# Kernel tuning notes

Hardware: AMD Instinct MI355X
Metric: run time of the kernel (lower is better)

The kernel has to match this reference:

```python
import jax, jax.numpy as jnp
import numpy as np

BUCKETS = 256
B, CIN, H, W = 16, 64, 128, 128
COUT, K = 64, 3


def setup_inputs() -> dict:
    key = jax.random.key(0)
    k1, k2, k3, k4, k5 = jax.random.split(key, 5)
    x = jax.random.normal(k1, (B, CIN, H, W), dtype=jnp.float32)
    x_hash = jax.random.normal(k2, (B, CIN, H, W), dtype=jnp.float32)
    conv_weight = jax.random.normal(k3, (COUT, CIN, K, K), dtype=jnp.float32)
    hash_value = jnp.sort(jax.random.normal(k4, (BUCKETS,), dtype=jnp.float32))
    bias = jax.random.normal(k5, (COUT,), dtype=jnp.float32) * 0.1
    return {"x": x, "x_hash": x_hash, "conv_weight": conv_weight,
            "hash_value": hash_value, "bias": bias}


def _conv(x, w, b):
    # stride 1, padding 1 -> same spatial size (matches nn.Conv2d(padding=1))
    y = jax.lax.conv_general_dilated(
        x, w, window_strides=(1, 1), padding=[(1, 1), (1, 1)],
        dimension_numbers=("NCHW", "OIHW", "NCHW"))
    return y + b[None, :, None, None]


def _hash_weights(conv_weight, hash_value):
    # Uniform bucketization of weights into BUCKETS bins over [min, max],
    # then gather of the learned per-bucket hash value.
    w_min = jnp.min(conv_weight)
    w_max = jnp.max(conv_weight)
    width = (w_max - w_min) / BUCKETS
    idx = jnp.floor((conv_weight - w_min) / width).astype(jnp.int32)
    # w == max floors to BUCKETS; torch code assigns it the last bucket.
    idx = jnp.clip(idx, 0, BUCKETS - 1)
    return jnp.take(hash_value, idx)


def reference(x, x_hash, conv_weight, hash_value, bias):
    hash_weight = _hash_weights(conv_weight, hash_value)
    out = _conv(x, conv_weight, bias)
    hash_out = _conv(x, hash_weight, bias)
    out_hash = _conv(x_hash, hash_weight, bias)
    return (out, hash_out, out_hash)
```

## Files before the change

### kernel.cpp

```cpp
#include <hip/hip_runtime.h>
#include <stdint.h>

typedef short short8_t __attribute__((ext_vector_type(8)));
typedef unsigned short ushort2_t __attribute__((ext_vector_type(2)));
typedef float f32x4    __attribute__((ext_vector_type(4)));

__device__ __forceinline__ unsigned short f2bf(float f) {
  unsigned int u = __float_as_uint(f);
  u += 0x7FFFu + ((u >> 16) & 1u);
  return (unsigned short)(u >> 16);
}

__device__ __forceinline__ void glld16(const void* src, char* lds) {
  __builtin_amdgcn_global_load_lds(
      (const __attribute__((address_space(1))) void*)src,
      (__attribute__((address_space(3))) void*)lds, 16, 0, 0);
}

__device__ __forceinline__ short8_t lds_rd(const char* smem, int a) {
  int aa = a ^ (((a >> 7) & 7) << 4);
  return *(const short8_t*)(smem + aa);
}

__global__ __launch_bounds__(256) void minmax_kernel(const float* __restrict__ w,
                                                     float* __restrict__ mm) {
  int tid = threadIdx.x;
  float mn = 1e30f, mx = -1e30f;
  const float4* w4 = (const float4*)w;
  for (int i = tid; i < 9216; i += 256) {
    float4 v = w4[i];
    mn = fminf(mn, fminf(fminf(v.x, v.y), fminf(v.z, v.w)));
    mx = fmaxf(mx, fmaxf(fmaxf(v.x, v.y), fmaxf(v.z, v.w)));
  }
  for (int off = 32; off; off >>= 1) {
    mn = fminf(mn, __shfl_down(mn, off));
    mx = fmaxf(mx, __shfl_down(mx, off));
  }
  __shared__ float smn[4], smx[4];
  if ((tid & 63) == 0) { smn[tid >> 6] = mn; smx[tid >> 6] = mx; }
  __syncthreads();
  if (tid == 0) {
    mn = fminf(fminf(smn[0], smn[1]), fminf(smn[2], smn[3]));
    mx = fmaxf(fmaxf(smx[0], smx[1]), fmaxf(smx[2], smx[3]));
    mm[0] = mn; mm[1] = mx;
  }
}

__global__ __launch_bounds__(256) void hashprep_kernel(const float* __restrict__ w,
                                                       const float* __restrict__ hv,
                                                       const float* __restrict__ mm,
                                                       unsigned short* __restrict__ w0,
                                                       unsigned short* __restrict__ w1) {
  int t = blockIdx.x * 256 + threadIdx.x;
  if (t >= 36864) return;
  float mn = mm[0], mx = mm[1];
  float width = (mx - mn) / 256.0f;
  float wv = w[t];
  int idx = min(max((int)floorf((wv - mn) / width), 0), 255);
  float hw = hv[idx];
  int co  = t / 576;
  int rem = t - co * 576;
  int ci  = rem / 9;
  int tap = rem - ci * 9;
  int mt = co >> 4, m = co & 15;
  int ks = ci >> 5, g = (ci & 31) >> 3, e = ci & 7;
  int dst = ((tap * 8 + mt * 2 + ks) * 64 + g * 16 + m) * 8 + e;
  w0[dst] = f2bf(wv);
  w1[dst] = f2bf(hw);
}

__global__ __launch_bounds__(256) void xprep_kernel(const float* __restrict__ x,
                                                    unsigned short* __restrict__ xbf) {
  __shared__ unsigned short T[64 * 130];
  int t  = threadIdx.x;
  int bh = blockIdx.x;
  int b = bh >> 7, h = bh & 127;
  const f32x4* x4 = (const f32x4*)x;
  size_t xrow = (((size_t)(b * 64) * 128 + h) << 5);
  #pragma unroll
  for (int k = 0; k < 8; ++k) {
    int j = k * 256 + t;
    int c = j >> 5, w4 = j & 31;
    f32x4 v = x4[xrow + ((size_t)c << 12) + w4];
    ushort2_t lo, hi;
    lo[0] = f2bf(v[0]); lo[1] = f2bf(v[1]);
    hi[0] = f2bf(v[2]); hi[1] = f2bf(v[3]);
    *(ushort2_t*)&T[c * 130 + w4 * 4]     = lo;
    *(ushort2_t*)&T[c * 130 + w4 * 4 + 2] = hi;
  }
  __syncthreads();
  size_t rb = (size_t)bh * (130 * 64);
  if (t < 16) {
    short8_t z = {0, 0, 0, 0, 0, 0, 0, 0};
    int col = (t < 8) ? 0 : 129, ch = t & 7;
    *(short8_t*)(xbf + rb + col * 64 + ch * 8) = z;
  }
  #pragma unroll
  for (int k = 0; k < 4; ++k) {
    int q = k * 256 + t;
    int w = q >> 3, o8 = (q & 7) * 8;
    short8_t v;
    #pragma unroll
    for (int j = 0; j < 8; ++j) v[j] = (short)T[(o8 + j) * 130 + w];
    *(short8_t*)(xbf + rb + (size_t)(w + 1) * 64 + o8) = v;
  }
}

#define XR 8448

template<int NSETS>
__global__ __launch_bounds__(256, 2) void conv_kernel(
    const unsigned short* __restrict__ xbf,
    const char* __restrict__ zeropage,
    const unsigned short* __restrict__ wf0,
    const unsigned short* __restrict__ wf1,
    const float* __restrict__ bias,
    float* __restrict__ out0,
    float* __restrict__ out1) {

  __shared__ char smem[6 * XR];

  int tid = threadIdx.x, lane = tid & 63, wv = tid >> 6;
  int m = lane & 15, g = lane >> 4;

  int bx0 = blockIdx.x;
  int bx  = (bx0 & 7) * 128 + (bx0 >> 3);
  int b = bx >> 6, rowblk = (bx >> 1) & 31, wblk = bx & 1;
  int h0 = rowblk * 4, W0 = wblk * 64;

  const unsigned short* wsrc[2] = {wf0, wf1};

  short8_t aw[NSETS][8];
  #pragma unroll
  for (int s = 0; s < NSETS; ++s)
    #pragma unroll
    for (int i = 0; i < 8; ++i)
      aw[s][i] = *(const short8_t*)(wsrc[s] + i * 512 + lane * 8);

  const char* xb = (const char*)xbf + (size_t)b * (130 * 128 * 128) + (size_t)W0 * 128;
  for (int batch = wv; batch < 50; batch += 4) {
    int q = batch * 64 + lane;
    if (q < 3168) {
      int r = q / 528;
      int o = (q - r * 528) << 4;
      int swz = o ^ (((q >> 3) & 7) << 4);
      int hin = h0 + r - 1;
      const char* src = ((unsigned)hin < 128u) ? (xb + (size_t)hin * 16640 + swz)
                                               : (zeropage + swz);
      glld16(src, smem + batch * 1024);
    }
  }

  f32x4 acc[NSETS][4][4];
  #pragma unroll
  for (int s = 0; s < NSETS; ++s)
    #pragma unroll
    for (int i = 0; i < 4; ++i)
      #pragma unroll
      for (int j = 0; j < 4; ++j) acc[s][i][j] = (f32x4){0.f, 0.f, 0.f, 0.f};

  int bcol[4];
  #pragma unroll
  for (int nf = 0; nf < 4; ++nf) bcol[nf] = ((nf * 16 + m) << 7) + (g << 4);

  __syncthreads();

  #pragma unroll
  for (int t = 0; t < 9; ++t) {
    if (t) {
      #pragma unroll
      for (int s = 0; s < NSETS; ++s)
        #pragma unroll
        for (int i = 0; i < 8; ++i)
          aw[s][i] = *(const short8_t*)(wsrc[s] + t * 4096 + i * 512 + lane * 8);
    }
    int kh = t / 3, kw = t - kh * 3;
    int xtap = (wv + kh) * XR + (kw << 7);
    #pragma unroll
    for (int ks = 0; ks < 2; ++ks) {
      short8_t bf[4];
      #pragma unroll
      for (int nf = 0; nf < 4; ++nf) bf[nf] = lds_rd(smem, xtap + bcol[nf] + (ks << 6));
      #pragma unroll
      for (int s = 0; s < NSETS; ++s)
        #pragma unroll
        for (int mt = 0; mt < 4; ++mt)
          #pragma unroll
          for (int nf = 0; nf < 4; ++nf)
            acc[s][mt][nf] = __builtin_amdgcn_mfma_f32_16x16x32_bf16(
                aw[s][mt * 2 + ks], bf[nf], acc[s][mt][nf], 0, 0, 0);
    }
  }

  size_t ob = (size_t)b * 64 * 16384 + (size_t)(h0 + wv) * 128 + W0;
  #pragma unroll
  for (int s = 0; s < NSETS; ++s) {
    float* op = s ? out1 : out0;
    #pragma unroll
    for (int mt = 0; mt < 4; ++mt)
      #pragma unroll
      for (int r4 = 0; r4 < 4; ++r4) {
        int co = mt * 16 + g * 4 + r4;
        float bv = bias[co];
        #pragma unroll
        for (int nf = 0; nf < 4; ++nf)
          op[ob + (size_t)co * 16384 + nf * 16 + m] = acc[s][mt][nf][r4] + bv;
      }
  }
}

extern "C" void kernel_launch(void* const* d_in, const int* in_sizes, int n_in,
                              void* d_out, int out_size, void* d_ws, size_t ws_size,
                              hipStream_t stream) {
  const float* x    = (const float*)d_in[0];
  const float* xh   = (const float*)d_in[1];
  const float* cw   = (const float*)d_in[2];
  const float* hv   = (const float*)d_in[3];
  const float* bias = (const float*)d_in[4];

  float* out      = (float*)d_out;
  float* hash_out = out + 16777216;
  float* out_hash = out + 33554432;

  char* ws = (char*)d_ws;
  float* mm            = (float*)ws;
  char* zeropage       = ws + 128;
  unsigned short* w0F  = (unsigned short*)(ws + 32768);
  unsigned short* w1F  = (unsigned short*)(ws + 32768 + 73728);
  unsigned short* xbf  = (unsigned short*)(ws + 180224);

  hipMemsetAsync(zeropage, 0, 16640, stream);
  minmax_kernel<<<1, 256, 0, stream>>>(cw, mm);
  hashprep_kernel<<<144, 256, 0, stream>>>(cw, hv, mm, w0F, w1F);

  xprep_kernel<<<2048, 256, 0, stream>>>(x, xbf);
  conv_kernel<2><<<1024, 256, 0, stream>>>(xbf, zeropage, w0F, w1F, bias, out, hash_out);
  xprep_kernel<<<2048, 256, 0, stream>>>(xh, xbf);
  conv_kernel<1><<<1024, 256, 0, stream>>>(xbf, zeropage, w1F, w1F, bias, out_hash, out_hash);
}
```

Baseline: 392.0 us.

## Merge conv launches, use 32x32x16 MFMA, and swizzle the xprep transpose

Both inputs are converted in a single xprep launch into separate bf16 buffers, and one conv launch of 2048 blocks covers both passes, with each block choosing two weight sets or one. The MFMA tile changes from 16x16x32 to 32x32x16, and the weight fragment layout is rebuilt to match. The xprep transpose now uses an XOR-swizzled LDS tile with packed channel pairs and vector reads. This removes two launches and the serial dependency between the passes, and should cut LDS operand reads per MFMA. The cost is extra workspace for a second bf16 buffer, uneven work across blocks, and possible register-pressure changes from the runtime branch on the number of weight sets.

```diff
diff --git a/kernel.cpp b/kernel.cpp
--- a/kernel.cpp
+++ b/kernel.cpp
@@ -2,8 +2,8 @@
 #include <stdint.h>
 
 typedef short short8_t __attribute__((ext_vector_type(8)));
-typedef unsigned short ushort2_t __attribute__((ext_vector_type(2)));
 typedef float f32x4    __attribute__((ext_vector_type(4)));
+typedef float f32x16   __attribute__((ext_vector_type(16)));
 
 __device__ __forceinline__ unsigned short f2bf(float f) {
   unsigned int u = __float_as_uint(f);
@@ -62,82 +62,102 @@
   int rem = t - co * 576;
   int ci  = rem / 9;
   int tap = rem - ci * 9;
-  int mt = co >> 4, m = co & 15;
-  int ks = ci >> 5, g = (ci & 31) >> 3, e = ci & 7;
-  int dst = ((tap * 8 + mt * 2 + ks) * 64 + g * 16 + m) * 8 + e;
+  int mt = co >> 5, m = co & 31;
+  int ks = ci >> 4, k = ci & 15;
+  int f = mt * 4 + ks;
+  int lane = (k >> 3) * 32 + m;
+  int dst = ((tap * 8 + f) * 64 + lane) * 8 + (k & 7);
   w0[dst] = f2bf(wv);
   w1[dst] = f2bf(hw);
 }
 
 __global__ __launch_bounds__(256) void xprep_kernel(const float* __restrict__ x,
-                                                    unsigned short* __restrict__ xbf) {
-  __shared__ unsigned short T[64 * 130];
-  int t  = threadIdx.x;
-  int bh = blockIdx.x;
+                                                    const float* __restrict__ xh,
+                                                    unsigned short* __restrict__ xbf,
+                                                    unsigned short* __restrict__ xhbf) {
+  __shared__ unsigned short T[128 * 64];
+  int t   = threadIdx.x;
+  int bid = blockIdx.x;
+  int which = bid >> 11;
+  int bh = bid & 2047;
+  const float* src = which ? xh : x;
+  unsigned short* dst = which ? xhbf : xbf;
   int b = bh >> 7, h = bh & 127;
-  const f32x4* x4 = (const f32x4*)x;
+  const f32x4* x4 = (const f32x4*)src;
   size_t xrow = (((size_t)(b * 64) * 128 + h) << 5);
   #pragma unroll
-  for (int k = 0; k < 8; ++k) {
-    int j = k * 256 + t;
-    int c = j >> 5, w4 = j & 31;
-    f32x4 v = x4[xrow + ((size_t)c << 12) + w4];
-    ushort2_t lo, hi;
-    lo[0] = f2bf(v[0]); lo[1] = f2bf(v[1]);
-    hi[0] = f2bf(v[2]); hi[1] = f2bf(v[3]);
-    *(ushort2_t*)&T[c * 130 + w4 * 4]     = lo;
-    *(ushort2_t*)&T[c * 130 + w4 * 4 + 2] = hi;
+  for (int kk = 0; kk < 4; ++kk) {
+    int j = kk * 256 + t;
+    int c2 = j >> 5, w4 = j & 31;
+    int c = c2 * 2;
+    f32x4 v0 = x4[xrow + ((size_t)c << 12) + w4];
+    f32x4 v1 = x4[xrow + ((size_t)(c + 1) << 12) + w4];
+    int cs = c ^ ((w4 & 7) << 3);
+    #pragma unroll
+    for (int jj = 0; jj < 4; ++jj) {
+      int w = w4 * 4 + jj;
+      unsigned int pk = (unsigned int)f2bf(v0[jj]) | ((unsigned int)f2bf(v1[jj]) << 16);
+      *(unsigned int*)&T[w * 64 + cs] = pk;
+    }
   }
   __syncthreads();
   size_t rb = (size_t)bh * (130 * 64);
   if (t < 16) {
     short8_t z = {0, 0, 0, 0, 0, 0, 0, 0};
     int col = (t < 8) ? 0 : 129, ch = t & 7;
-    *(short8_t*)(xbf + rb + col * 64 + ch * 8) = z;
-  }
-  #pragma unroll
-  for (int k = 0; k < 4; ++k) {
-    int q = k * 256 + t;
-    int w = q >> 3, o8 = (q & 7) * 8;
-    short8_t v;
-    #pragma unroll
-    for (int j = 0; j < 8; ++j) v[j] = (short)T[(o8 + j) * 130 + w];
-    *(short8_t*)(xbf + rb + (size_t)(w + 1) * 64 + o8) = v;
+    *(short8_t*)(dst + rb + col * 64 + ch * 8) = z;
+  }
+  #pragma unroll
+  for (int kk = 0; kk < 4; ++kk) {
+    int q = kk * 256 + t;
+    int w = q >> 3, c0 = (q & 7) * 8;
+    int cs0 = c0 ^ (((w >> 2) & 7) << 3);
+    short8_t v = *(const short8_t*)&T[w * 64 + cs0];
+    *(short8_t*)(dst + rb + (size_t)(w + 1) * 64 + c0) = v;
   }
 }
 
 #define XR 8448
 
-template<int NSETS>
 __global__ __launch_bounds__(256, 2) void conv_kernel(
     const unsigned short* __restrict__ xbf,
+    const unsigned short* __restrict__ xhbf,
     const char* __restrict__ zeropage,
     const unsigned short* __restrict__ wf0,
     const unsigned short* __restrict__ wf1,
     const float* __restrict__ bias,
     float* __restrict__ out0,
-    float* __restrict__ out1) {
+    float* __restrict__ out1,
+    float* __restrict__ out2) {
 
   __shared__ char smem[6 * XR];
 
   int tid = threadIdx.x, lane = tid & 63, wv = tid >> 6;
-  int m = lane & 15, g = lane >> 4;
+  int nlo = lane & 31, hi = lane >> 5;
 
   int bx0 = blockIdx.x;
-  int bx  = (bx0 & 7) * 128 + (bx0 >> 3);
-  int b = bx >> 6, rowblk = (bx >> 1) & 31, wblk = bx & 1;
+  int bx  = (bx0 & 7) * 256 + (bx0 >> 3);
+  int which = bx >> 10;
+  int r10 = bx & 1023;
+  int b = r10 >> 6, rowblk = (r10 >> 1) & 31, wblk = r10 & 1;
   int h0 = rowblk * 4, W0 = wblk * 64;
-
-  const unsigned short* wsrc[2] = {wf0, wf1};
-
-  short8_t aw[NSETS][8];
-  #pragma unroll
-  for (int s = 0; s < NSETS; ++s)
+  int nsets = 2 - which;
+
+  const unsigned short* xsrc  = which ? xhbf : xbf;
+  const unsigned short* wsrc0 = which ? wf1 : wf0;
+  float* o0 = which ? out2 : out0;
+
+  short8_t aw0[8], aw1[8];
+  #pragma unroll
+  for (int i = 0; i < 8; ++i)
+    aw0[i] = *(const short8_t*)(wsrc0 + i * 512 + lane * 8);
+  if (nsets == 2) {
     #pragma unroll
     for (int i = 0; i < 8; ++i)
-      aw[s][i] = *(const short8_t*)(wsrc[s] + i * 512 + lane * 8);
-
-  const char* xb = (const char*)xbf + (size_t)b * (130 * 128 * 128) + (size_t)W0 * 128;
+      aw1[i] = *(const short8_t*)(wf1 + i * 512 + lane * 8);
+  }
+
+  const char* xb = (const char*)xsrc + (size_t)b * (130 * 128 * 128) + (size_t)W0 * 128;
   for (int batch = wv; batch < 50; batch += 4) {
     int q = batch * 64 + lane;
     if (q < 3168) {
@@ -151,17 +171,14 @@
     }
   }
 
-  f32x4 acc[NSETS][4][4];
-  #pragma unroll
-  for (int s = 0; s < NSETS; ++s)
-    #pragma unroll
-    for (int i = 0; i < 4; ++i)
-      #pragma unroll
-      for (int j = 0; j < 4; ++j) acc[s][i][j] = (f32x4){0.f, 0.f, 0.f, 0.f};
-
-  int bcol[4];
-  #pragma unroll
-  for (int nf = 0; nf < 4; ++nf) bcol[nf] = ((nf * 16 + m) << 7) + (g << 4);
+  f32x16 acc0[2][2], acc1[2][2];
+  #pragma unroll
+  for (int i = 0; i < 2; ++i)
+    #pragma unroll
+    for (int j = 0; j < 2; ++j) {
+      #pragma unroll
+      for (int e = 0; e < 16; ++e) { acc0[i][j][e] = 0.f; acc1[i][j][e] = 0.f; }
+    }
 
   __syncthreads();
 
@@ -169,43 +186,59 @@
   for (int t = 0; t < 9; ++t) {
     if (t) {
       #pragma unroll
-      for (int s = 0; s < NSETS; ++s)
+      for (int i = 0; i < 8; ++i)
+        aw0[i] = *(const short8_t*)(wsrc0 + t * 4096 + i * 512 + lane * 8);
+      if (nsets == 2) {
         #pragma unroll
         for (int i = 0; i < 8; ++i)
-          aw[s][i] = *(const short8_t*)(wsrc[s] + t * 4096 + i * 512 + lane * 8);
+          aw1[i] = *(const short8_t*)(wf1 + t * 4096 + i * 512 + lane * 8);
+      }
     }
     int kh = t / 3, kw = t - kh * 3;
-    int xtap = (wv + kh) * XR + (kw << 7);
-    #pragma unroll
-    for (int ks = 0; ks < 2; ++ks) {
-      short8_t bf[4];
-      #pragma unroll
-      for (int nf = 0; nf < 4; ++nf) bf[nf] = lds_rd(smem, xtap + bcol[nf] + (ks << 6));
-      #pragma unroll
-      for (int s = 0; s < NSETS; ++s)
-        #pragma unroll
-        for (int mt = 0; mt < 4; ++mt)
+    int xbase = (wv + kh) * XR + (kw << 7) + (hi << 4);
+    #pragma unroll
+    for (int ks = 0; ks < 4; ++ks) {
+      short8_t bf[2];
+      #pragma unroll
+      for (int nf = 0; nf < 2; ++nf)
+        bf[nf] = lds_rd(smem, xbase + ((nf * 32 + nlo) << 7) + (ks << 5));
+      #pragma unroll
+      for (int mt = 0; mt < 2; ++mt)
+        #pragma unroll
+        for (int nf = 0; nf < 2; ++nf)
+          acc0[mt][nf] = __builtin_amdgcn_mfma_f32_32x32x16_bf16(
+              aw0[mt * 4 + ks], bf[nf], acc0[mt][nf], 0, 0, 0);
+      if (nsets == 2) {
+        #pragma unroll
+        for (int mt = 0; mt < 2; ++mt)
           #pragma unroll
-          for (int nf = 0; nf < 4; ++nf)
-            acc[s][mt][nf] = __builtin_amdgcn_mfma_f32_16x16x32_bf16(
-                aw[s][mt * 2 + ks], bf[nf], acc[s][mt][nf], 0, 0, 0);
+          for (int nf = 0; nf < 2; ++nf)
+            acc1[mt][nf] = __builtin_amdgcn_mfma_f32_32x32x16_bf16(
+                aw1[mt * 4 + ks], bf[nf], acc1[mt][nf], 0, 0, 0);
+      }
     }
   }
 
   size_t ob = (size_t)b * 64 * 16384 + (size_t)(h0 + wv) * 128 + W0;
   #pragma unroll
-  for (int s = 0; s < NSETS; ++s) {
-    float* op = s ? out1 : out0;
-    #pragma unroll
-    for (int mt = 0; mt < 4; ++mt)
-      #pragma unroll
-      for (int r4 = 0; r4 < 4; ++r4) {
-        int co = mt * 16 + g * 4 + r4;
-        float bv = bias[co];
-        #pragma unroll
-        for (int nf = 0; nf < 4; ++nf)
-          op[ob + (size_t)co * 16384 + nf * 16 + m] = acc[s][mt][nf][r4] + bv;
+  for (int mt = 0; mt < 2; ++mt)
+    #pragma unroll
+    for (int nf = 0; nf < 2; ++nf)
+      #pragma unroll
+      for (int r = 0; r < 16; ++r) {
+        int co = mt * 32 + (r & 3) + 8 * (r >> 2) + 4 * hi;
+        o0[ob + (size_t)co * 16384 + nf * 32 + nlo] = acc0[mt][nf][r] + bias[co];
       }
+  if (nsets == 2) {
+    #pragma unroll
+    for (int mt = 0; mt < 2; ++mt)
+      #pragma unroll
+      for (int nf = 0; nf < 2; ++nf)
+        #pragma unroll
+        for (int r = 0; r < 16; ++r) {
+          int co = mt * 32 + (r & 3) + 8 * (r >> 2) + 4 * hi;
+          out1[ob + (size_t)co * 16384 + nf * 32 + nlo] = acc1[mt][nf][r] + bias[co];
+        }
   }
 }
 
@@ -226,15 +259,14 @@
   float* mm            = (float*)ws;
   char* zeropage       = ws + 128;
   unsigned short* w0F  = (unsigned short*)(ws + 32768);
-  unsigned short* w1F  = (unsigned short*)(ws + 32768 + 73728);
+  unsigned short* w1F  = (unsigned short*)(ws + 106496);
   unsigned short* xbf  = (unsigned short*)(ws + 180224);
+  unsigned short* xhbf = (unsigned short*)(ws + 180224 + 34078720);
 
   hipMemsetAsync(zeropage, 0, 16640, stream);
   minmax_kernel<<<1, 256, 0, stream>>>(cw, mm);
   hashprep_kernel<<<144, 256, 0, stream>>>(cw, hv, mm, w0F, w1F);
-
-  xprep_kernel<<<2048, 256, 0, stream>>>(x, xbf);
-  conv_kernel<2><<<1024, 256, 0, stream>>>(xbf, zeropage, w0F, w1F, bias, out, hash_out);
-  xprep_kernel<<<2048, 256, 0, stream>>>(xh, xbf);
-  conv_kernel<1><<<1024, 256, 0, stream>>>(xbf, zeropage, w1F, w1F, bias, out_hash, out_hash);
-}
+  xprep_kernel<<<4096, 256, 0, stream>>>(x, xh, xbf, xhbf);
+  conv_kernel<<<2048, 256, 0, stream>>>(xbf, xhbf, zeropage, w0F, w1F, bias,
+                                        out, hash_out, out_hash);
+}
```

Measured after the change: 394.6 us. About the same (+0.7%).
